# Performance work log

Measured on AMD Instinct MI355X. Metric: run time of the kernel, lower is better.

## Reference

```python
import jax, jax.numpy as jnp
import numpy as np

BLOCK = 8
C = 64


def setup_inputs() -> dict:
    key = jax.random.key(0)
    k = jax.random.split(key, 6)
    B, H, W = 4, 512, 512
    x = jax.random.normal(k[0], (B, C, H, W), jnp.float32)
    # per-channel 8x8 transform matrices (torch.randn init)
    tw = jax.random.normal(k[1], (C, BLOCK, BLOCK), jnp.float32)
    s = 1.0 / np.sqrt(C).astype(np.float32)
    w1 = jax.random.normal(k[2], (C, C), jnp.float32) * s  # 1x1 conv weight [out,in]
    b1 = jax.random.normal(k[3], (C,), jnp.float32) * s
    w2 = jax.random.normal(k[4], (C, C), jnp.float32) * s
    b2 = jax.random.normal(k[5], (C,), jnp.float32) * s
    return {"x": x, "tw": tw, "w1": w1, "b1": b1, "w2": w2, "b2": b2}


def reference(x, tw, w1, b1, w2, b2):
    B, Cc, H, W = x.shape
    bs = BLOCK
    nh, nw = H // bs, W // bs
    # extract 8x8 blocks: [b,c,nh,nw,i,j]
    p = x.reshape(B, Cc, nh, bs, nw, bs).transpose(0, 1, 2, 4, 3, 5)
    # per-channel T @ P @ T^T : out[p,q] = T[p,i] P[i,j] T[q,j]
    t = jnp.einsum('cpi,bcnmij,cqj->bcnmpq', tw, p, tw)
    # fold blocks back to image
    y = t.transpose(0, 1, 2, 4, 3, 5).reshape(B, Cc, H, W)
    # quantization gate: 1x1 conv -> relu -> 1x1 conv -> sigmoid
    g = jnp.einsum('oc,bchw->bohw', w1, y) + b1[None, :, None, None]
    g = jax.nn.relu(g)
    g = jnp.einsum('oc,bchw->bohw', w2, g) + b2[None, :, None, None]
    g = jax.nn.sigmoid(g)
    return y * g
```

## Files before the change

kernel.cpp:

```cpp
#include <hip/hip_runtime.h>

typedef float f4 __attribute__((ext_vector_type(4)));
typedef __attribute__((ext_vector_type(4))) float f32x4;
typedef _Float16 h8 __attribute__((ext_vector_type(8)));

__device__ __forceinline__ void gload_lds16(const float* g, float* l) {
    __builtin_amdgcn_global_load_lds(
        (const __attribute__((address_space(1))) void*)g,
        (__attribute__((address_space(3))) void*)l, 16, 0, 0);
}

#define BAR_LGKM()  do { asm volatile("s_waitcnt lgkmcnt(0)" ::: "memory"); \
    __builtin_amdgcn_s_barrier(); asm volatile("" ::: "memory"); } while (0)
#define BAR_VM8()   do { asm volatile("s_waitcnt vmcnt(8) lgkmcnt(0)" ::: "memory"); \
    __builtin_amdgcn_s_barrier(); asm volatile("" ::: "memory"); } while (0)
#define BAR_VM0()   do { asm volatile("s_waitcnt vmcnt(0) lgkmcnt(0)" ::: "memory"); \
    __builtin_amdgcn_s_barrier(); asm volatile("" ::: "memory"); } while (0)

__global__ __launch_bounds__(256, 2)
void avif_pipe4(const float* __restrict__ x, const float* __restrict__ twm,
                const float* __restrict__ w1, const float* __restrict__ b1,
                const float* __restrict__ w2, const float* __restrict__ b2,
                float* __restrict__ out)
{
    __shared__ float xs[8192];
    __shared__ ushort ysf[128][64];
    __shared__ ushort hsf[128][64];

    const int t = threadIdx.x;
    const int bid = blockIdx.x;
    const int wc  = bid >> 8;
    const int rem = bid & 255;
    const int hb  = rem & 63;
    const int b   = rem >> 6;

    const int wv = t >> 6, lane = t & 63;
    const int li = lane & 15, lg = lane >> 4, l7 = li & 7;
    const int lb3 = (li >> 3) << 2;

    const float* xslab = x + (((size_t)(b * 64)) * 512 + (size_t)hb * 8) * 512 + wc * 16;
    const float* gp[8];
#pragma unroll
    for (int j = 0; j < 8; ++j) {
        const int G = j * 256 + t;
        const int c = G >> 5;
        const int v = (G & 31) ^ (c & 7);
        const int r = v >> 2, qg = v & 3;
        gp[j] = xslab + (size_t)c * 262144 + r * 512 + qg * 4;
    }
    float* lbase = &xs[wv * 256];

    h8 w1f[2], w2f[2];
    {
        const float* p1 = w1 + (16 * wv + li) * 64 + lg * 8;
        const float* p2 = w2 + (16 * wv + li) * 64 + lg * 8;
#pragma unroll
        for (int kk = 0; kk < 2; ++kk) {
            f4 a = *(const f4*)(p1 + kk * 32);
            f4 d = *(const f4*)(p1 + kk * 32 + 4);
            h8 f;
#pragma unroll
            for (int q = 0; q < 4; ++q) { f[q] = (_Float16)a[q]; f[4 + q] = (_Float16)d[q]; }
            w1f[kk] = f;
            a = *(const f4*)(p2 + kk * 32);
            d = *(const f4*)(p2 + kk * 32 + 4);
#pragma unroll
            for (int q = 0; q < 4; ++q) { f[q] = (_Float16)a[q]; f[4 + q] = (_Float16)d[q]; }
            w2f[kk] = f;
        }
    }
    const int o0 = 16 * wv + 4 * lg;
    const f4 b1v = *(const f4*)(b1 + o0);
    const float b2s = b2[16 * wv + li];
    const int sg0 = ((lg       ^ l7 ^ lb3) << 3);
    const int sg1 = (((4 + lg) ^ l7 ^ lb3) << 3);
    const int go  = o0 >> 3, co = 4 * (lg & 1);
    const int ch  = 16 * wv + li;
    const int cgE = ch >> 3, c7E = li & 7;

    const int pid = t >> 1, h2 = t & 1;
    const int c   = pid & 63, blk = pid >> 6, Q0 = 4 * h2;
    const float* tB = twm + c * 64;
    const int sc = c * 128, swc = c & 7;
    const int cg = c >> 3, c7 = c & 7;

#pragma unroll
    for (int j = 0; j < 8; ++j) gload_lds16(gp[j], lbase + j * 1024);
    BAR_VM0();

    for (int tile = 0; tile < 16; ++tile) {
        const int wt = 2 * tile + wc;

        {
            float M[8][4];
            {
                f4 Ph[8];
#pragma unroll
                for (int i = 0; i < 8; ++i)
                    Ph[i] = *(const f4*)&xs[sc + ((i * 4 + blk * 2) ^ swc) * 4];
#pragma unroll
                for (int qq = 0; qq < 4; ++qq) {
                    f4 Th = *(const f4*)(tB + (Q0 + qq) * 8);
#pragma unroll
                    for (int i = 0; i < 8; ++i) {
                        float s = Ph[i][0] * Th[0];
                        s = fmaf(Ph[i][1], Th[1], s);
                        s = fmaf(Ph[i][2], Th[2], s);
                        s = fmaf(Ph[i][3], Th[3], s);
                        M[i][qq] = s;
                    }
                }
#pragma unroll
                for (int i = 0; i < 8; ++i)
                    Ph[i] = *(const f4*)&xs[sc + ((i * 4 + blk * 2 + 1) ^ swc) * 4];
#pragma unroll
                for (int qq = 0; qq < 4; ++qq) {
                    f4 Th = *(const f4*)(tB + (Q0 + qq) * 8 + 4);
#pragma unroll
                    for (int i = 0; i < 8; ++i) {
                        float s = M[i][qq];
                        s = fmaf(Ph[i][0], Th[0], s);
                        s = fmaf(Ph[i][1], Th[1], s);
                        s = fmaf(Ph[i][2], Th[2], s);
                        s = fmaf(Ph[i][3], Th[3], s);
                        M[i][qq] = s;
                    }
                }
            }
#pragma unroll
            for (int p = 0; p < 8; ++p) {
                f4 a = *(const f4*)(tB + p * 8);
                f4 d = *(const f4*)(tB + p * 8 + 4);
                const int px0 = p * 16 + blk * 8;
#pragma unroll
                for (int qq = 0; qq < 4; ++qq) {
                    const int q = Q0 + qq;
                    float s = a[0] * M[0][qq];
                    s = fmaf(a[1], M[1][qq], s);
                    s = fmaf(a[2], M[2][qq], s);
                    s = fmaf(a[3], M[3][qq], s);
                    s = fmaf(d[0], M[4][qq], s);
                    s = fmaf(d[1], M[5][qq], s);
                    s = fmaf(d[2], M[6][qq], s);
                    s = fmaf(d[3], M[7][qq], s);
                    const int idx = ((cg ^ q ^ (blk << 2)) << 3) | c7;
                    *(_Float16*)&ysf[px0 + q][idx] = (_Float16)s;
                }
            }
        }
        BAR_LGKM();

        if (tile < 15) {
#pragma unroll
            for (int j = 0; j < 8; ++j)
                gload_lds16(gp[j] + (tile + 1) * 32, lbase + j * 1024);
        }

        f32x4 acc[8];
#pragma unroll
        for (int j = 0; j < 8; ++j) acc[j] = (f32x4){0.f, 0.f, 0.f, 0.f};
#pragma unroll
        for (int j = 0; j < 8; ++j) {
            const int row = 16 * j + li;
            h8 bh0 = *(const h8*)&ysf[row][sg0];
            h8 bh1 = *(const h8*)&ysf[row][sg1];
            acc[j] = __builtin_amdgcn_mfma_f32_16x16x32_f16(w1f[0], bh0, acc[j], 0, 0, 0);
            acc[j] = __builtin_amdgcn_mfma_f32_16x16x32_f16(w1f[1], bh1, acc[j], 0, 0, 0);
        }
#pragma unroll
        for (int j = 0; j < 8; ++j) {
            const int px = 16 * j + li;
            const int idx = ((go ^ l7 ^ lb3) << 3) + co;
            union { _Float16 h[2]; unsigned u; } p01, p23;
            p01.h[0] = (_Float16)fmaxf(acc[j][0] + b1v[0], 0.f);
            p01.h[1] = (_Float16)fmaxf(acc[j][1] + b1v[1], 0.f);
            p23.h[0] = (_Float16)fmaxf(acc[j][2] + b1v[2], 0.f);
            p23.h[1] = (_Float16)fmaxf(acc[j][3] + b1v[3], 0.f);
            *(unsigned*)&hsf[px][idx]     = p01.u;
            *(unsigned*)&hsf[px][idx + 2] = p23.u;
        }
        BAR_LGKM();

#pragma unroll
        for (int j = 0; j < 8; ++j) acc[j] = (f32x4){0.f, 0.f, 0.f, 0.f};
#pragma unroll
        for (int j = 0; j < 8; ++j) {
            const int row = 16 * j + li;
            h8 ah0 = *(const h8*)&hsf[row][sg0];
            h8 ah1 = *(const h8*)&hsf[row][sg1];
            acc[j] = __builtin_amdgcn_mfma_f32_16x16x32_f16(ah0, w2f[0], acc[j], 0, 0, 0);
            acc[j] = __builtin_amdgcn_mfma_f32_16x16x32_f16(ah1, w2f[1], acc[j], 0, 0, 0);
        }
        float* oB = out + ((size_t)(b * 64) + ch) * 262144
                    + (size_t)(hb * 8) * 512 + wt * 16 + 4 * lg;
#pragma unroll
        for (int j = 0; j < 8; ++j) {
            f4 r;
#pragma unroll
            for (int r4 = 0; r4 < 4; ++r4) {
                const int pc = 4 * lg + r4;
                const int px = 16 * j + pc;
                const int idx = ((cgE ^ (pc & 7) ^ (((pc >> 3) & 1) << 2)) << 3) | c7E;
                float yv = (float)(*(const _Float16*)&ysf[px][idx]);
                float z = acc[j][r4] + b2s;
                float g = __builtin_amdgcn_rcpf(1.f + __expf(-z));
                r[r4] = yv * g;
            }
            *(f4*)(oB + (size_t)j * 512) = r;
        }
        BAR_VM8();
    }
}

extern "C" void kernel_launch(void* const* d_in, const int* in_sizes, int n_in,
                              void* d_out, int out_size, void* d_ws, size_t ws_size,
                              hipStream_t stream) {
    (void)in_sizes; (void)n_in; (void)out_size; (void)d_ws; (void)ws_size;
    const float* x   = (const float*)d_in[0];
    const float* twm = (const float*)d_in[1];
    const float* w1  = (const float*)d_in[2];
    const float* b1  = (const float*)d_in[3];
    const float* w2  = (const float*)d_in[4];
    const float* b2  = (const float*)d_in[5];
    float* out = (float*)d_out;

    avif_pipe4<<<dim3(512), dim3(256), 0, stream>>>(x, twm, w1, b1, w2, b2, out);
}
```

Baseline: 193.5 us.

## Double-buffer transformed tile and software-pipeline block transform with MFMA gating

Makes the ysf buffer double-buffered and moves the per-channel 8x8 transform of the next tile to the end of the current iteration, after the output stores. The intent is to overlap transform ALU work with the MFMA gate stages and outstanding global stores, and to drop one barrier per tile. The barrier between the two MFMA stages now waits on vmcnt(0), which also drains the in-flight output stores. LDS use grows by 16 KB, which may limit occupancy.

```diff
diff --git a/kernel.cpp b/kernel.cpp
--- a/kernel.cpp
+++ b/kernel.cpp
@@ -10,21 +10,19 @@
         (__attribute__((address_space(3))) void*)l, 16, 0, 0);
 }
 
-#define BAR_LGKM()  do { asm volatile("s_waitcnt lgkmcnt(0)" ::: "memory"); \
+#define BAR_VM() do { asm volatile("s_waitcnt vmcnt(0) lgkmcnt(0)" ::: "memory"); \
     __builtin_amdgcn_s_barrier(); asm volatile("" ::: "memory"); } while (0)
-#define BAR_VM8()   do { asm volatile("s_waitcnt vmcnt(8) lgkmcnt(0)" ::: "memory"); \
+#define BAR_LG() do { asm volatile("s_waitcnt lgkmcnt(0)" ::: "memory"); \
     __builtin_amdgcn_s_barrier(); asm volatile("" ::: "memory"); } while (0)
-#define BAR_VM0()   do { asm volatile("s_waitcnt vmcnt(0) lgkmcnt(0)" ::: "memory"); \
-    __builtin_amdgcn_s_barrier(); asm volatile("" ::: "memory"); } while (0)
 
 __global__ __launch_bounds__(256, 2)
-void avif_pipe4(const float* __restrict__ x, const float* __restrict__ twm,
+void avif_pipe5(const float* __restrict__ x, const float* __restrict__ twm,
                 const float* __restrict__ w1, const float* __restrict__ b1,
                 const float* __restrict__ w2, const float* __restrict__ b2,
                 float* __restrict__ out)
 {
     __shared__ float xs[8192];
-    __shared__ ushort ysf[128][64];
+    __shared__ ushort ysf[2][128][64];
     __shared__ ushort hsf[128][64];
 
     const int t = threadIdx.x;
@@ -84,71 +82,74 @@
     const int sc = c * 128, swc = c & 7;
     const int cg = c >> 3, c7 = c & 7;
 
+    auto transform = [&](int buf) {
+        float M[8][4];
+        {
+            f4 Ph[8];
+#pragma unroll
+            for (int i = 0; i < 8; ++i)
+                Ph[i] = *(const f4*)&xs[sc + ((i * 4 + blk * 2) ^ swc) * 4];
+#pragma unroll
+            for (int qq = 0; qq < 4; ++qq) {
+                f4 Th = *(const f4*)(tB + (Q0 + qq) * 8);
+#pragma unroll
+                for (int i = 0; i < 8; ++i) {
+                    float s = Ph[i][0] * Th[0];
+                    s = fmaf(Ph[i][1], Th[1], s);
+                    s = fmaf(Ph[i][2], Th[2], s);
+                    s = fmaf(Ph[i][3], Th[3], s);
+                    M[i][qq] = s;
+                }
+            }
+#pragma unroll
+            for (int i = 0; i < 8; ++i)
+                Ph[i] = *(const f4*)&xs[sc + ((i * 4 + blk * 2 + 1) ^ swc) * 4];
+#pragma unroll
+            for (int qq = 0; qq < 4; ++qq) {
+                f4 Th = *(const f4*)(tB + (Q0 + qq) * 8 + 4);
+#pragma unroll
+                for (int i = 0; i < 8; ++i) {
+                    float s = M[i][qq];
+                    s = fmaf(Ph[i][0], Th[0], s);
+                    s = fmaf(Ph[i][1], Th[1], s);
+                    s = fmaf(Ph[i][2], Th[2], s);
+                    s = fmaf(Ph[i][3], Th[3], s);
+                    M[i][qq] = s;
+                }
+            }
+        }
+#pragma unroll
+        for (int p = 0; p < 8; ++p) {
+            f4 a = *(const f4*)(tB + p * 8);
+            f4 d = *(const f4*)(tB + p * 8 + 4);
+            const int px0 = p * 16 + blk * 8;
+#pragma unroll
+            for (int qq = 0; qq < 4; ++qq) {
+                const int q = Q0 + qq;
+                float s = a[0] * M[0][qq];
+                s = fmaf(a[1], M[1][qq], s);
+                s = fmaf(a[2], M[2][qq], s);
+                s = fmaf(a[3], M[3][qq], s);
+                s = fmaf(d[0], M[4][qq], s);
+                s = fmaf(d[1], M[5][qq], s);
+                s = fmaf(d[2], M[6][qq], s);
+                s = fmaf(d[3], M[7][qq], s);
+                const int idx = ((cg ^ q ^ (blk << 2)) << 3) | c7;
+                *(_Float16*)&ysf[buf][px0 + q][idx] = (_Float16)s;
+            }
+        }
+    };
+
 #pragma unroll
     for (int j = 0; j < 8; ++j) gload_lds16(gp[j], lbase + j * 1024);
-    BAR_VM0();
-
+    BAR_VM();
+    transform(0);
+    BAR_LG();
+
+#pragma unroll 1
     for (int tile = 0; tile < 16; ++tile) {
-        const int wt = 2 * tile + wc;
-
-        {
-            float M[8][4];
-            {
-                f4 Ph[8];
-#pragma unroll
-                for (int i = 0; i < 8; ++i)
-                    Ph[i] = *(const f4*)&xs[sc + ((i * 4 + blk * 2) ^ swc) * 4];
-#pragma unroll
-                for (int qq = 0; qq < 4; ++qq) {
-                    f4 Th = *(const f4*)(tB + (Q0 + qq) * 8);
-#pragma unroll
-                    for (int i = 0; i < 8; ++i) {
-                        float s = Ph[i][0] * Th[0];
-                        s = fmaf(Ph[i][1], Th[1], s);
-                        s = fmaf(Ph[i][2], Th[2], s);
-                        s = fmaf(Ph[i][3], Th[3], s);
-                        M[i][qq] = s;
-                    }
-                }
-#pragma unroll
-                for (int i = 0; i < 8; ++i)
-                    Ph[i] = *(const f4*)&xs[sc + ((i * 4 + blk * 2 + 1) ^ swc) * 4];
-#pragma unroll
-                for (int qq = 0; qq < 4; ++qq) {
-                    f4 Th = *(const f4*)(tB + (Q0 + qq) * 8 + 4);
-#pragma unroll
-                    for (int i = 0; i < 8; ++i) {
-                        float s = M[i][qq];
-                        s = fmaf(Ph[i][0], Th[0], s);
-                        s = fmaf(Ph[i][1], Th[1], s);
-                        s = fmaf(Ph[i][2], Th[2], s);
-                        s = fmaf(Ph[i][3], Th[3], s);
-                        M[i][qq] = s;
-                    }
-                }
-            }
-#pragma unroll
-            for (int p = 0; p < 8; ++p) {
-                f4 a = *(const f4*)(tB + p * 8);
-                f4 d = *(const f4*)(tB + p * 8 + 4);
-                const int px0 = p * 16 + blk * 8;
-#pragma unroll
-                for (int qq = 0; qq < 4; ++qq) {
-                    const int q = Q0 + qq;
-                    float s = a[0] * M[0][qq];
-                    s = fmaf(a[1], M[1][qq], s);
-                    s = fmaf(a[2], M[2][qq], s);
-                    s = fmaf(a[3], M[3][qq], s);
-                    s = fmaf(d[0], M[4][qq], s);
-                    s = fmaf(d[1], M[5][qq], s);
-                    s = fmaf(d[2], M[6][qq], s);
-                    s = fmaf(d[3], M[7][qq], s);
-                    const int idx = ((cg ^ q ^ (blk << 2)) << 3) | c7;
-                    *(_Float16*)&ysf[px0 + q][idx] = (_Float16)s;
-                }
-            }
-        }
-        BAR_LGKM();
+        const int buf = tile & 1;
+        const int wt  = 2 * tile + wc;
 
         if (tile < 15) {
 #pragma unroll
@@ -162,8 +163,8 @@
 #pragma unroll
         for (int j = 0; j < 8; ++j) {
             const int row = 16 * j + li;
-            h8 bh0 = *(const h8*)&ysf[row][sg0];
-            h8 bh1 = *(const h8*)&ysf[row][sg1];
+            h8 bh0 = *(const h8*)&ysf[buf][row][sg0];
+            h8 bh1 = *(const h8*)&ysf[buf][row][sg1];
             acc[j] = __builtin_amdgcn_mfma_f32_16x16x32_f16(w1f[0], bh0, acc[j], 0, 0, 0);
             acc[j] = __builtin_amdgcn_mfma_f32_16x16x32_f16(w1f[1], bh1, acc[j], 0, 0, 0);
         }
@@ -179,7 +180,7 @@
             *(unsigned*)&hsf[px][idx]     = p01.u;
             *(unsigned*)&hsf[px][idx + 2] = p23.u;
         }
-        BAR_LGKM();
+        BAR_VM();
 
 #pragma unroll
         for (int j = 0; j < 8; ++j) acc[j] = (f32x4){0.f, 0.f, 0.f, 0.f};
@@ -201,14 +202,16 @@
                 const int pc = 4 * lg + r4;
                 const int px = 16 * j + pc;
                 const int idx = ((cgE ^ (pc & 7) ^ (((pc >> 3) & 1) << 2)) << 3) | c7E;
-                float yv = (float)(*(const _Float16*)&ysf[px][idx]);
+                float yv = (float)(*(const _Float16*)&ysf[buf][px][idx]);
                 float z = acc[j][r4] + b2s;
                 float g = __builtin_amdgcn_rcpf(1.f + __expf(-z));
                 r[r4] = yv * g;
             }
             *(f4*)(oB + (size_t)j * 512) = r;
         }
-        BAR_VM8();
+        if (tile < 15) transform(buf ^ 1);
+
+        if (tile < 15) BAR_LG();
     }
 }
 
@@ -224,5 +227,5 @@
     const float* b2  = (const float*)d_in[5];
     float* out = (float*)d_out;
 
-    avif_pipe4<<<dim3(512), dim3(256), 0, stream>>>(x, twm, w1, b1, w2, b2, out);
+    avif_pipe5<<<dim3(512), dim3(256), 0, stream>>>(x, twm, w1, b1, w2, b2, out);
 }
```

Result: faster. 181.5 us (-6.2%).
